# Kernel tuning notes

Hardware: AMD Instinct MI355X
Metric: run time of the kernel (lower is better)

The kernel has to match this reference:

```python
import jax, jax.numpy as jnp
import numpy as np

B, C, H, W = 8, 512, 32, 32
HEADS = 8
GROUPS = 32
EPS = 1e-5


def setup_inputs() -> dict:
    key = jax.random.key(0)
    ks = jax.random.split(key, 7)
    x = jax.random.normal(ks[0], (B, C, H, W), dtype=jnp.float32)
    gamma = jnp.ones((C,), dtype=jnp.float32)
    beta = jnp.zeros((C,), dtype=jnp.float32)
    w_qkv = jax.random.normal(ks[1], (3 * C, C), dtype=jnp.float32) * 0.02
    b_qkv = jnp.zeros((3 * C,), dtype=jnp.float32)
    # NOTE: original zero-inits proj; we use small random weights so the
    # attention path contributes to the output (zero proj => out == x).
    w_proj = jax.random.normal(ks[2], (C, C), dtype=jnp.float32) * 0.02
    b_proj = jnp.zeros((C,), dtype=jnp.float32)
    return {"x": x, "gamma": gamma, "beta": beta, "w_qkv": w_qkv,
            "b_qkv": b_qkv, "w_proj": w_proj, "b_proj": b_proj}


def group_norm(x, gamma, beta):
    b, c, h, w = x.shape
    xg = x.reshape(b, GROUPS, -1)
    mu = xg.mean(axis=-1, keepdims=True)
    var = xg.var(axis=-1, keepdims=True)
    xn = ((xg - mu) * jax.lax.rsqrt(var + EPS)).reshape(b, c, h, w)
    return xn * gamma[:, None, None] + beta[:, None, None]


def reference(x, gamma, beta, w_qkv, b_qkv, w_proj, b_proj):
    b, c, h, w = x.shape
    hd = c // HEADS
    n = h * w
    hn = group_norm(x, gamma, beta).reshape(b, c, n)        # [B,C,N]
    # 1x1 conv == channel matmul
    qkv = jnp.einsum('oc,bcn->bon', w_qkv, hn) + b_qkv[:, None]
    qkv = qkv.reshape(b, 3, HEADS, hd, n)
    q, k, v = qkv[:, 0], qkv[:, 1], qkv[:, 2]               # [B,H,hd,N]
    scale = hd ** -0.5
    scores = jnp.einsum('bhci,bhcj->bhij', q, k) * scale    # [B,H,N,N]
    attn = jax.nn.softmax(scores, axis=-1)                  # stable (max-sub)
    out = jnp.einsum('bhij,bhcj->bhci', attn, v).reshape(b, c, n)
    proj = jnp.einsum('oc,bcn->bon', w_proj, out) + b_proj[:, None]
    return x + proj.reshape(b, c, h, w)
```

## Files before the change

kernel.cpp:

```cpp
#include <hip/hip_runtime.h>
#include <math.h>

#define Bn 8
#define Cc 512
#define HW 1024
#define HEADS 8
#define HD 64
#define GROUPS 32
#define CPG 16
#define EPS 1e-5f

typedef float f32x4 __attribute__((ext_vector_type(4)));
typedef __bf16 bf16x8 __attribute__((ext_vector_type(8)));
typedef __bf16 bf16x4 __attribute__((ext_vector_type(4)));
typedef short s16x4 __attribute__((ext_vector_type(4)));
typedef unsigned u32x2 __attribute__((ext_vector_type(2)));

__device__ __forceinline__ void async16(const __bf16* g, __bf16* l) {
    __builtin_amdgcn_global_load_lds((const __attribute__((address_space(1))) unsigned int*)g,
                                     (__attribute__((address_space(3))) unsigned int*)l, 16, 0, 0);
}

__device__ __forceinline__ f32x4 mfma16(bf16x4 a, bf16x4 b, f32x4 c) {
    return __builtin_amdgcn_mfma_f32_16x16x16bf16_1k(
        __builtin_bit_cast(s16x4, a), __builtin_bit_cast(s16x4, b), c, 0, 0, 0);
}

__device__ __forceinline__ unsigned pk_bf16(float f1, float f0) {
    return __builtin_amdgcn_perm(__builtin_bit_cast(unsigned, f1),
                                 __builtin_bit_cast(unsigned, f0), 0x07060302u);
}

__global__ void conv_kernel(const float* __restrict__ a, __bf16* __restrict__ da, int na4,
                            const float* __restrict__ b, __bf16* __restrict__ db, int nb4) {
    int i = blockIdx.x * 256 + threadIdx.x;
    if (i < na4) {
        float4 v = ((const float4*)a)[i];
        bf16x4 o = { (__bf16)v.x, (__bf16)v.y, (__bf16)v.z, (__bf16)v.w };
        ((bf16x4*)da)[i] = o;
    } else {
        int j = i - na4;
        if (j < nb4) {
            float4 v = ((const float4*)b)[j];
            bf16x4 o = { (__bf16)v.x, (__bf16)v.y, (__bf16)v.z, (__bf16)v.w };
            ((bf16x4*)db)[j] = o;
        }
    }
}

__global__ __launch_bounds__(256) void gn_stats(const float* __restrict__ x,
                                                float* __restrict__ gstats) {
    int bg = blockIdx.x;
    int b = bg >> 5, g = bg & 31;
    const float* xp = x + ((size_t)b * Cc + g * CPG) * HW;
    int tid = threadIdx.x;
    float s = 0.f, ss = 0.f;
    for (int i = tid; i < CPG * HW; i += 256) {
        float v = xp[i];
        s += v; ss += v * v;
    }
    __shared__ float red0[4], red1[4];
    for (int off = 32; off > 0; off >>= 1) {
        s  += __shfl_down(s, off);
        ss += __shfl_down(ss, off);
    }
    int wave = tid >> 6, lane = tid & 63;
    if (lane == 0) { red0[wave] = s; red1[wave] = ss; }
    __syncthreads();
    if (tid == 0) {
        float S  = red0[0] + red0[1] + red0[2] + red0[3];
        float SS = red1[0] + red1[1] + red1[2] + red1[3];
        float mean = S / (float)(CPG * HW);
        float var  = SS / (float)(CPG * HW) - mean * mean;
        gstats[bg * 2]     = mean;
        gstats[bg * 2 + 1] = rsqrtf(var + EPS);
    }
}

__global__ __launch_bounds__(256) void gn_apply(const float* __restrict__ x,
                                                const float* __restrict__ gamma,
                                                const float* __restrict__ beta,
                                                const float* __restrict__ gstats,
                                                __bf16* __restrict__ hnT) {
    int b = blockIdx.y, n0 = blockIdx.x * 32;
    __shared__ __align__(16) __bf16 T[32 * 520];
    __shared__ float gl[512], bl[512], sm[32], sr[32];
    int tid = threadIdx.x;
    if (tid < 32) {
        sm[tid] = gstats[(b * 32 + tid) * 2];
        sr[tid] = gstats[(b * 32 + tid) * 2 + 1];
    }
    for (int i = tid; i < 512; i += 256) { gl[i] = gamma[i]; bl[i] = beta[i]; }
    __syncthreads();
    const float* xb = x + (size_t)b * Cc * HW + n0;
    for (int i = tid; i < 16384; i += 256) {
        int c = i >> 5, n = i & 31;
        float v = xb[(size_t)c * HW + n];
        int g = c >> 4;
        T[n * 520 + c] = (__bf16)((v - sm[g]) * sr[g] * gl[c] + bl[c]);
    }
    __syncthreads();
    __bf16* hb = hnT + ((size_t)b * HW + n0) * Cc;
    for (int j = tid; j < 2048; j += 256) {
        int n = j >> 6, ch = j & 63;
        *(bf16x8*)&hb[(size_t)n * Cc + ch * 8] = *(const bf16x8*)&T[n * 520 + ch * 8];
    }
}

__global__ __launch_bounds__(256) void qkv_gemm(
    const __bf16* __restrict__ hnT, const __bf16* __restrict__ wq,
    const float* __restrict__ bias, __bf16* __restrict__ qkT,
    __bf16* __restrict__ vbuf, float scaleLo) {
    __shared__ __align__(16) __bf16 As[128 * 64];
    __shared__ __align__(16) __bf16 Bs[128 * 64];
    int tid = threadIdx.x;
    int wv = tid >> 6, lane = tid & 63, ln = lane & 15, quad = lane >> 4;
    int b = blockIdx.z;
    bool isQK = blockIdx.y < 8;
    int bm = (isQK ? blockIdx.y : blockIdx.y - 8) * 128;
    int bn = blockIdx.x * 128;
    const __bf16* hb = hnT + (size_t)b * HW * Cc;
    const __bf16* Pb = isQK ? hb : wq + (size_t)1024 * 512;
    const __bf16* Qb = isQK ? wq : hb;
    int wm = (wv >> 1) * 64, wn = (wv & 1) * 64;

    f32x4 acc[4][4];
    #pragma unroll
    for (int i = 0; i < 4; ++i)
        #pragma unroll
        for (int j = 0; j < 4; ++j) acc[i][j] = (f32x4){0.f, 0.f, 0.f, 0.f};

    for (int k0 = 0; k0 < 512; k0 += 64) {
        __syncthreads();
        #pragma unroll
        for (int u = 0; u < 4; ++u) {
            int idx = u * 256 + tid;
            int r = idx >> 3, lc = idx & 7;
            int cg = lc ^ (r & 7);
            async16(Pb + (size_t)(bm + r) * 512 + k0 + cg * 8, &As[r * 64 + lc * 8]);
            async16(Qb + (size_t)(bn + r) * 512 + k0 + cg * 8, &Bs[r * 64 + lc * 8]);
        }
        __syncthreads();
        bf16x8 af[4][2], bff[4][2];
        #pragma unroll
        for (int mt = 0; mt < 4; ++mt) {
            int row = wm + mt * 16 + ln;
            #pragma unroll
            for (int h = 0; h < 2; ++h) {
                int cc = (h * 4 + quad) ^ (ln & 7);
                af[mt][h] = *(const bf16x8*)&As[row * 64 + cc * 8];
            }
        }
        #pragma unroll
        for (int nt = 0; nt < 4; ++nt) {
            int row = wn + nt * 16 + ln;
            #pragma unroll
            for (int h = 0; h < 2; ++h) {
                int cc = (h * 4 + quad) ^ (ln & 7);
                bff[nt][h] = *(const bf16x8*)&Bs[row * 64 + cc * 8];
            }
        }
        #pragma unroll
        for (int mt = 0; mt < 4; ++mt)
            #pragma unroll
            for (int nt = 0; nt < 4; ++nt) {
                acc[mt][nt] = __builtin_amdgcn_mfma_f32_16x16x32_bf16(af[mt][0], bff[nt][0], acc[mt][nt], 0, 0, 0);
                acc[mt][nt] = __builtin_amdgcn_mfma_f32_16x16x32_bf16(af[mt][1], bff[nt][1], acc[mt][nt], 0, 0, 0);
            }
    }

    if (isQK) {
        __bf16* out = qkT + (size_t)b * HW * 1024;
        float bcol[4], scol[4];
        #pragma unroll
        for (int nt = 0; nt < 4; ++nt) {
            int col = bn + wn + nt * 16 + ln;
            bcol[nt] = bias[col];
            scol[nt] = (col < 512) ? scaleLo : 1.0f;
        }
        #pragma unroll
        for (int mt = 0; mt < 4; ++mt)
            #pragma unroll
            for (int r = 0; r < 4; ++r) {
                int row = bm + wm + mt * 16 + quad * 4 + r;
                #pragma unroll
                for (int nt = 0; nt < 4; ++nt) {
                    int col = bn + wn + nt * 16 + ln;
                    out[(size_t)row * 1024 + col] = (__bf16)((acc[mt][nt][r] + bcol[nt]) * scol[nt]);
                }
            }
    } else {
        __bf16* out = vbuf + (size_t)b * Cc * HW;
        #pragma unroll
        for (int mt = 0; mt < 4; ++mt)
            #pragma unroll
            for (int r = 0; r < 4; ++r) {
                int row = bm + wm + mt * 16 + quad * 4 + r;
                float brow = bias[1024 + row];
                #pragma unroll
                for (int nt = 0; nt < 4; ++nt) {
                    int col = bn + wn + nt * 16 + ln;
                    out[(size_t)row * 1024 + col] = (__bf16)(acc[mt][nt][r] + brow);
                }
            }
    }
}

__global__ __launch_bounds__(256) void proj_gemm(
    const __bf16* __restrict__ wp, const __bf16* __restrict__ attnT,
    const float* __restrict__ bias, const float* __restrict__ resid,
    float* __restrict__ outp) {
    __shared__ __align__(16) __bf16 As[64 * 64];
    __shared__ __align__(16) __bf16 Bs[128 * 64];
    int tid = threadIdx.x;
    int wv = tid >> 6, lane = tid & 63, ln = lane & 15, quad = lane >> 4;
    int b = blockIdx.z;
    int bm = blockIdx.y * 64, bn = blockIdx.x * 128;
    const __bf16* Qb = attnT + (size_t)b * HW * Cc;
    int wm = (wv >> 1) * 32, wn = (wv & 1) * 64;

    f32x4 acc[2][4];
    #pragma unroll
    for (int i = 0; i < 2; ++i)
        #pragma unroll
        for (int j = 0; j < 4; ++j) acc[i][j] = (f32x4){0.f, 0.f, 0.f, 0.f};

    for (int k0 = 0; k0 < 512; k0 += 64) {
        __syncthreads();
        #pragma unroll
        for (int u = 0; u < 2; ++u) {
            int idx = u * 256 + tid;
            int r = idx >> 3, lc = idx & 7;
            int cg = lc ^ (r & 7);
            async16(wp + (size_t)(bm + r) * 512 + k0 + cg * 8, &As[r * 64 + lc * 8]);
        }
        #pragma unroll
        for (int u = 0; u < 4; ++u) {
            int idx = u * 256 + tid;
            int r = idx >> 3, lc = idx & 7;
            int cg = lc ^ (r & 7);
            async16(Qb + (size_t)(bn + r) * 512 + k0 + cg * 8, &Bs[r * 64 + lc * 8]);
        }
        __syncthreads();
        bf16x8 af[2][2], bff[4][2];
        #pragma unroll
        for (int mt = 0; mt < 2; ++mt) {
            int row = wm + mt * 16 + ln;
            #pragma unroll
            for (int h = 0; h < 2; ++h) {
                int cc = (h * 4 + quad) ^ (ln & 7);
                af[mt][h] = *(const bf16x8*)&As[row * 64 + cc * 8];
            }
        }
        #pragma unroll
        for (int nt = 0; nt < 4; ++nt) {
            int row = wn + nt * 16 + ln;
            #pragma unroll
            for (int h = 0; h < 2; ++h) {
                int cc = (h * 4 + quad) ^ (ln & 7);
                bff[nt][h] = *(const bf16x8*)&Bs[row * 64 + cc * 8];
            }
        }
        #pragma unroll
        for (int mt = 0; mt < 2; ++mt)
            #pragma unroll
            for (int nt = 0; nt < 4; ++nt) {
                acc[mt][nt] = __builtin_amdgcn_mfma_f32_16x16x32_bf16(af[mt][0], bff[nt][0], acc[mt][nt], 0, 0, 0);
                acc[mt][nt] = __builtin_amdgcn_mfma_f32_16x16x32_bf16(af[mt][1], bff[nt][1], acc[mt][nt], 0, 0, 0);
            }
    }

    float* out = outp + (size_t)b * Cc * HW;
    const float* res = resid + (size_t)b * Cc * HW;
    #pragma unroll
    for (int mt = 0; mt < 2; ++mt)
        #pragma unroll
        for (int r = 0; r < 4; ++r) {
            int row = bm + wm + mt * 16 + quad * 4 + r;
            float bv = bias[row];
            #pragma unroll
            for (int nt = 0; nt < 4; ++nt) {
                int col = bn + wn + nt * 16 + ln;
                size_t idx = (size_t)row * 1024 + col;
                out[idx] = acc[mt][nt][r] + bv + res[idx];
            }
        }
}

__global__ __launch_bounds__(256) void attn_mfma(const __bf16* __restrict__ qkT,
                                                 const __bf16* __restrict__ vbuf,
                                                 __bf16* __restrict__ attnT) {
    __shared__ __align__(16) __bf16 Ks[2][64 * 64];
    __shared__ __align__(16) __bf16 Vs[2][64 * 64];
    int tid = threadIdx.x;
    int wv = tid >> 6, lane = tid & 63, ln = lane & 15, quad = lane >> 4;
    int h = blockIdx.x, b = blockIdx.z;
    int i0 = blockIdx.y * 128 + wv * 32;

    const __bf16* qbase = qkT + ((size_t)b * HW + i0 + ln) * 1024 + h * HD + quad * 8;
    bf16x8 qf[2][2];
    #pragma unroll
    for (int mt = 0; mt < 2; ++mt) {
        qf[mt][0] = *(const bf16x8*)(qbase + (size_t)mt * 16 * 1024);
        qf[mt][1] = *(const bf16x8*)(qbase + (size_t)mt * 16 * 1024 + 32);
    }

    f32x4 oacc[2][4];
    #pragma unroll
    for (int mt = 0; mt < 2; ++mt)
        #pragma unroll
        for (int ct = 0; ct < 4; ++ct) oacc[mt][ct] = (f32x4){0.f, 0.f, 0.f, 0.f};
    float lsum[2] = {0.f, 0.f};

    for (int kt = 0; kt < 8; ++kt) {
        __syncthreads();
        #pragma unroll
        for (int hh = 0; hh < 2; ++hh) {
            int kb = kt * 128 + hh * 64;
            #pragma unroll
            for (int u = 0; u < 2; ++u) {
                int idx = u * 256 + tid;
                int r = idx >> 3, lc = idx & 7;
                int cg = lc ^ (r & 7);
                async16(qkT + ((size_t)b * HW + kb + r) * 1024 + 512 + h * HD + cg * 8,
                        &Ks[hh][idx * 8]);
                async16(vbuf + ((size_t)b * Cc + h * HD + r) * HW + kb + cg * 8,
                        &Vs[hh][idx * 8]);
            }
        }
        __syncthreads();

        #pragma unroll
        for (int hh = 0; hh < 2; ++hh) {
            f32x4 st[2][4];
            #pragma unroll
            for (int jt = 0; jt < 4; ++jt) {
                int row = jt * 16 + ln;
                int c0 = quad ^ (ln & 7);
                int c1 = (4 + quad) ^ (ln & 7);
                bf16x8 kf0 = *(const bf16x8*)&Ks[hh][row * 64 + c0 * 8];
                bf16x8 kf1 = *(const bf16x8*)&Ks[hh][row * 64 + c1 * 8];
                #pragma unroll
                for (int mt = 0; mt < 2; ++mt) {
                    f32x4 s = (f32x4){0.f, 0.f, 0.f, 0.f};
                    s = __builtin_amdgcn_mfma_f32_16x16x32_bf16(kf0, qf[mt][0], s, 0, 0, 0);
                    s = __builtin_amdgcn_mfma_f32_16x16x32_bf16(kf1, qf[mt][1], s, 0, 0, 0);
                    st[mt][jt] = s;
                }
            }

            bf16x4 pk[2][4];
            #pragma unroll
            for (int mt = 0; mt < 2; ++mt)
                #pragma unroll
                for (int jt = 0; jt < 4; ++jt) {
                    float p0 = __builtin_amdgcn_exp2f(st[mt][jt][0]);
                    float p1 = __builtin_amdgcn_exp2f(st[mt][jt][1]);
                    float p2 = __builtin_amdgcn_exp2f(st[mt][jt][2]);
                    float p3 = __builtin_amdgcn_exp2f(st[mt][jt][3]);
                    lsum[mt] += (p0 + p1) + (p2 + p3);
                    u32x2 w = { pk_bf16(p1, p0), pk_bf16(p3, p2) };
                    pk[mt][jt] = __builtin_bit_cast(bf16x4, w);
                }

            #pragma unroll
            for (int ct = 0; ct < 4; ++ct) {
                int row = ct * 16 + ln;
                bf16x4 vf[4];
                #pragma unroll
                for (int kss = 0; kss < 4; ++kss) {
                    int cc16 = (kss * 2 + (quad >> 1)) ^ (ln & 7);
                    vf[kss] = *(const bf16x4*)&Vs[hh][row * 64 + cc16 * 8 + (quad & 1) * 4];
                }
                #pragma unroll
                for (int mt = 0; mt < 2; ++mt)
                    #pragma unroll
                    for (int kss = 0; kss < 4; ++kss)
                        oacc[mt][ct] = mfma16(vf[kss], pk[mt][kss], oacc[mt][ct]);
            }
        }
    }

    #pragma unroll
    for (int mt = 0; mt < 2; ++mt) {
        lsum[mt] += __shfl_xor(lsum[mt], 16);
        lsum[mt] += __shfl_xor(lsum[mt], 32);
        float rl = 1.f / lsum[mt];
        __bf16* op = attnT + ((size_t)b * HW + i0 + mt * 16 + ln) * Cc + h * HD + quad * 4;
        #pragma unroll
        for (int ct = 0; ct < 4; ++ct) {
            bf16x4 o = { (__bf16)(oacc[mt][ct][0] * rl), (__bf16)(oacc[mt][ct][1] * rl),
                         (__bf16)(oacc[mt][ct][2] * rl), (__bf16)(oacc[mt][ct][3] * rl) };
            *(bf16x4*)(op + ct * 16) = o;
        }
    }
}

extern "C" void kernel_launch(void* const* d_in, const int* in_sizes, int n_in,
                              void* d_out, int out_size, void* d_ws, size_t ws_size,
                              hipStream_t stream) {
    const float* x      = (const float*)d_in[0];
    const float* gamma  = (const float*)d_in[1];
    const float* beta   = (const float*)d_in[2];
    const float* w_qkv  = (const float*)d_in[3];
    const float* b_qkv  = (const float*)d_in[4];
    const float* w_proj = (const float*)d_in[5];
    const float* b_proj = (const float*)d_in[6];
    float* out = (float*)d_out;

    __bf16* wq_bf  = (__bf16*)d_ws;
    __bf16* wp_bf  = wq_bf + (size_t)1536 * 512;
    __bf16* hnT    = wp_bf + (size_t)512 * 512;
    __bf16* qkT    = hnT + (size_t)Bn * HW * Cc;
    __bf16* vbuf   = qkT + (size_t)Bn * HW * 1024;
    __bf16* attnT  = vbuf + (size_t)Bn * Cc * HW;
    float*  gstats = (float*)(attnT + (size_t)Bn * HW * Cc);

    conv_kernel<<<1024, 256, 0, stream>>>(w_qkv, wq_bf, 196608, w_proj, wp_bf, 65536);

    gn_stats<<<Bn * GROUPS, 256, 0, stream>>>(x, gstats);
    dim3 gga(32, Bn);
    gn_apply<<<gga, 256, 0, stream>>>(x, gamma, beta, gstats, hnT);

    const float QSCALE = 0.125f * 1.44269504088896f;
    dim3 gqkv(8, 12, Bn);
    qkv_gemm<<<gqkv, 256, 0, stream>>>(hnT, wq_bf, b_qkv, qkT, vbuf, QSCALE);

    dim3 ga(8, 8, 8);
    attn_mfma<<<ga, 256, 0, stream>>>(qkT, vbuf, attnT);

    dim3 gp(8, 8, Bn);
    proj_gemm<<<gp, 256, 0, stream>>>(wp_bf, attnT, b_proj, x, out);
}
```

Before: 161.1 us.

## Fuse weight conversion with GN stats and halve attention query tile per block

```diff
diff --git a/kernel.cpp b/kernel.cpp
--- a/kernel.cpp
+++ b/kernel.cpp
@@ -31,29 +31,30 @@
                                  __builtin_bit_cast(unsigned, f0), 0x07060302u);
 }
 
-__global__ void conv_kernel(const float* __restrict__ a, __bf16* __restrict__ da, int na4,
-                            const float* __restrict__ b, __bf16* __restrict__ db, int nb4) {
-    int i = blockIdx.x * 256 + threadIdx.x;
-    if (i < na4) {
-        float4 v = ((const float4*)a)[i];
-        bf16x4 o = { (__bf16)v.x, (__bf16)v.y, (__bf16)v.z, (__bf16)v.w };
-        ((bf16x4*)da)[i] = o;
-    } else {
-        int j = i - na4;
-        if (j < nb4) {
-            float4 v = ((const float4*)b)[j];
+__global__ __launch_bounds__(256) void pre_kernel(const float* __restrict__ x,
+                                                  float* __restrict__ gstats,
+                                                  const float* __restrict__ wq,
+                                                  __bf16* __restrict__ wq_bf,
+                                                  const float* __restrict__ wp,
+                                                  __bf16* __restrict__ wp_bf) {
+    int blk = blockIdx.x;
+    int tid = threadIdx.x;
+    if (blk >= 256) {
+        int i = (blk - 256) * 256 + tid;
+        if (i < 196608) {
+            float4 v = ((const float4*)wq)[i];
             bf16x4 o = { (__bf16)v.x, (__bf16)v.y, (__bf16)v.z, (__bf16)v.w };
-            ((bf16x4*)db)[j] = o;
-        }
-    }
-}
-
-__global__ __launch_bounds__(256) void gn_stats(const float* __restrict__ x,
-                                                float* __restrict__ gstats) {
-    int bg = blockIdx.x;
-    int b = bg >> 5, g = bg & 31;
+            ((bf16x4*)wq_bf)[i] = o;
+        } else {
+            int j = i - 196608;
+            float4 v = ((const float4*)wp)[j];
+            bf16x4 o = { (__bf16)v.x, (__bf16)v.y, (__bf16)v.z, (__bf16)v.w };
+            ((bf16x4*)wp_bf)[j] = o;
+        }
+        return;
+    }
+    int b = blk >> 5, g = blk & 31;
     const float* xp = x + ((size_t)b * Cc + g * CPG) * HW;
-    int tid = threadIdx.x;
     float s = 0.f, ss = 0.f;
     for (int i = tid; i < CPG * HW; i += 256) {
         float v = xp[i];
@@ -72,8 +73,8 @@
         float SS = red1[0] + red1[1] + red1[2] + red1[3];
         float mean = S / (float)(CPG * HW);
         float var  = SS / (float)(CPG * HW) - mean * mean;
-        gstats[bg * 2]     = mean;
-        gstats[bg * 2 + 1] = rsqrtf(var + EPS);
+        gstats[blk * 2]     = mean;
+        gstats[blk * 2 + 1] = rsqrtf(var + EPS);
     }
 }
 
@@ -295,22 +296,16 @@
     int tid = threadIdx.x;
     int wv = tid >> 6, lane = tid & 63, ln = lane & 15, quad = lane >> 4;
     int h = blockIdx.x, b = blockIdx.z;
-    int i0 = blockIdx.y * 128 + wv * 32;
+    int i0 = blockIdx.y * 64 + wv * 16;
 
     const __bf16* qbase = qkT + ((size_t)b * HW + i0 + ln) * 1024 + h * HD + quad * 8;
-    bf16x8 qf[2][2];
+    bf16x8 qf0 = *(const bf16x8*)qbase;
+    bf16x8 qf1 = *(const bf16x8*)(qbase + 32);
+
+    f32x4 oacc[4];
     #pragma unroll
-    for (int mt = 0; mt < 2; ++mt) {
-        qf[mt][0] = *(const bf16x8*)(qbase + (size_t)mt * 16 * 1024);
-        qf[mt][1] = *(const bf16x8*)(qbase + (size_t)mt * 16 * 1024 + 32);
-    }
-
-    f32x4 oacc[2][4];
-    #pragma unroll
-    for (int mt = 0; mt < 2; ++mt)
-        #pragma unroll
-        for (int ct = 0; ct < 4; ++ct) oacc[mt][ct] = (f32x4){0.f, 0.f, 0.f, 0.f};
-    float lsum[2] = {0.f, 0.f};
+    for (int ct = 0; ct < 4; ++ct) oacc[ct] = (f32x4){0.f, 0.f, 0.f, 0.f};
+    float lsum = 0.f;
 
     for (int kt = 0; kt < 8; ++kt) {
         __syncthreads();
@@ -332,7 +327,7 @@
 
         #pragma unroll
         for (int hh = 0; hh < 2; ++hh) {
-            f32x4 st[2][4];
+            f32x4 st[4];
             #pragma unroll
             for (int jt = 0; jt < 4; ++jt) {
                 int row = jt * 16 + ln;
@@ -340,28 +335,23 @@
                 int c1 = (4 + quad) ^ (ln & 7);
                 bf16x8 kf0 = *(const bf16x8*)&Ks[hh][row * 64 + c0 * 8];
                 bf16x8 kf1 = *(const bf16x8*)&Ks[hh][row * 64 + c1 * 8];
-                #pragma unroll
-                for (int mt = 0; mt < 2; ++mt) {
-                    f32x4 s = (f32x4){0.f, 0.f, 0.f, 0.f};
-                    s = __builtin_amdgcn_mfma_f32_16x16x32_bf16(kf0, qf[mt][0], s, 0, 0, 0);
-                    s = __builtin_amdgcn_mfma_f32_16x16x32_bf16(kf1, qf[mt][1], s, 0, 0, 0);
-                    st[mt][jt] = s;
-                }
-            }
-
-            bf16x4 pk[2][4];
-            #pragma unroll
-            for (int mt = 0; mt < 2; ++mt)
-                #pragma unroll
-                for (int jt = 0; jt < 4; ++jt) {
-                    float p0 = __builtin_amdgcn_exp2f(st[mt][jt][0]);
-                    float p1 = __builtin_amdgcn_exp2f(st[mt][jt][1]);
-                    float p2 = __builtin_amdgcn_exp2f(st[mt][jt][2]);
-                    float p3 = __builtin_amdgcn_exp2f(st[mt][jt][3]);
-                    lsum[mt] += (p0 + p1) + (p2 + p3);
-                    u32x2 w = { pk_bf16(p1, p0), pk_bf16(p3, p2) };
-                    pk[mt][jt] = __builtin_bit_cast(bf16x4, w);
-                }
+                f32x4 s = (f32x4){0.f, 0.f, 0.f, 0.f};
+                s = __builtin_amdgcn_mfma_f32_16x16x32_bf16(kf0, qf0, s, 0, 0, 0);
+                s = __builtin_amdgcn_mfma_f32_16x16x32_bf16(kf1, qf1, s, 0, 0, 0);
+                st[jt] = s;
+            }
+
+            bf16x4 pk[4];
+            #pragma unroll
+            for (int jt = 0; jt < 4; ++jt) {
+                float p0 = __builtin_amdgcn_exp2f(st[jt][0]);
+                float p1 = __builtin_amdgcn_exp2f(st[jt][1]);
+                float p2 = __builtin_amdgcn_exp2f(st[jt][2]);
+                float p3 = __builtin_amdgcn_exp2f(st[jt][3]);
+                lsum += (p0 + p1) + (p2 + p3);
+                u32x2 w = { pk_bf16(p1, p0), pk_bf16(p3, p2) };
+                pk[jt] = __builtin_bit_cast(bf16x4, w);
+            }
 
             #pragma unroll
             for (int ct = 0; ct < 4; ++ct) {
@@ -373,26 +363,21 @@
                     vf[kss] = *(const bf16x4*)&Vs[hh][row * 64 + cc16 * 8 + (quad & 1) * 4];
                 }
                 #pragma unroll
-                for (int mt = 0; mt < 2; ++mt)
-                    #pragma unroll
-                    for (int kss = 0; kss < 4; ++kss)
-                        oacc[mt][ct] = mfma16(vf[kss], pk[mt][kss], oacc[mt][ct]);
-            }
-        }
-    }
-
+                for (int kss = 0; kss < 4; ++kss)
+                    oacc[ct] = mfma16(vf[kss], pk[kss], oacc[ct]);
+            }
+        }
+    }
+
+    lsum += __shfl_xor(lsum, 16);
+    lsum += __shfl_xor(lsum, 32);
+    float rl = 1.f / lsum;
+    __bf16* op = attnT + ((size_t)b * HW + i0 + ln) * Cc + h * HD + quad * 4;
     #pragma unroll
-    for (int mt = 0; mt < 2; ++mt) {
-        lsum[mt] += __shfl_xor(lsum[mt], 16);
-        lsum[mt] += __shfl_xor(lsum[mt], 32);
-        float rl = 1.f / lsum[mt];
-        __bf16* op = attnT + ((size_t)b * HW + i0 + mt * 16 + ln) * Cc + h * HD + quad * 4;
-        #pragma unroll
-        for (int ct = 0; ct < 4; ++ct) {
-            bf16x4 o = { (__bf16)(oacc[mt][ct][0] * rl), (__bf16)(oacc[mt][ct][1] * rl),
-                         (__bf16)(oacc[mt][ct][2] * rl), (__bf16)(oacc[mt][ct][3] * rl) };
-            *(bf16x4*)(op + ct * 16) = o;
-        }
+    for (int ct = 0; ct < 4; ++ct) {
+        bf16x4 o = { (__bf16)(oacc[ct][0] * rl), (__bf16)(oacc[ct][1] * rl),
+                     (__bf16)(oacc[ct][2] * rl), (__bf16)(oacc[ct][3] * rl) };
+        *(bf16x4*)(op + ct * 16) = o;
     }
 }
 
@@ -416,9 +401,8 @@
     __bf16* attnT  = vbuf + (size_t)Bn * Cc * HW;
     float*  gstats = (float*)(attnT + (size_t)Bn * HW * Cc);
 
-    conv_kernel<<<1024, 256, 0, stream>>>(w_qkv, wq_bf, 196608, w_proj, wp_bf, 65536);
-
-    gn_stats<<<Bn * GROUPS, 256, 0, stream>>>(x, gstats);
+    pre_kernel<<<1280, 256, 0, stream>>>(x, gstats, w_qkv, wq_bf, w_proj, wp_bf);
+
     dim3 gga(32, Bn);
     gn_apply<<<gga, 256, 0, stream>>>(x, gamma, beta, gstats, hnT);
 
@@ -426,7 +410,7 @@
     dim3 gqkv(8, 12, Bn);
     qkv_gemm<<<gqkv, 256, 0, stream>>>(hnT, wq_bf, b_qkv, qkT, vbuf, QSCALE);
 
-    dim3 ga(8, 8, 8);
+    dim3 ga(8, 16, 8);
     attn_mfma<<<ga, 256, 0, stream>>>(qkT, vbuf, attnT);
 
     dim3 gp(8, 8, Bn);
```

Result: no change. 164.0 us (+1.8%).

## Fuse weight conversion, group-norm stats and apply into one kernel

Applied to the files above, without the earlier changes.

```diff
diff --git a/kernel.cpp b/kernel.cpp
--- a/kernel.cpp
+++ b/kernel.cpp
@@ -31,35 +31,46 @@
                                  __builtin_bit_cast(unsigned, f0), 0x07060302u);
 }
 
-__global__ void conv_kernel(const float* __restrict__ a, __bf16* __restrict__ da, int na4,
-                            const float* __restrict__ b, __bf16* __restrict__ db, int nb4) {
-    int i = blockIdx.x * 256 + threadIdx.x;
-    if (i < na4) {
-        float4 v = ((const float4*)a)[i];
+__global__ __launch_bounds__(256) void gn_fused(const float* __restrict__ x,
+                                                const float* __restrict__ gamma,
+                                                const float* __restrict__ beta,
+                                                __bf16* __restrict__ hnT,
+                                                const float* __restrict__ wq,
+                                                __bf16* __restrict__ wq_bf,
+                                                const float* __restrict__ wp,
+                                                __bf16* __restrict__ wp_bf) {
+    int blk = blockIdx.x;
+    int tid = threadIdx.x;
+    if (blk >= 256) {
+        int i = (blk - 256) * 256 + tid;
+        if (i < 196608) {
+            float4 v = ((const float4*)wq)[i];
+            bf16x4 o = { (__bf16)v.x, (__bf16)v.y, (__bf16)v.z, (__bf16)v.w };
+            ((bf16x4*)wq_bf)[i] = o;
+        } else {
+            int j = i - 196608;
+            float4 v = ((const float4*)wp)[j];
+            bf16x4 o = { (__bf16)v.x, (__bf16)v.y, (__bf16)v.z, (__bf16)v.w };
+            ((bf16x4*)wp_bf)[j] = o;
+        }
+        return;
+    }
+    int b = blk >> 5, g = blk & 31;
+    const float* xp = x + ((size_t)b * Cc + g * CPG) * HW;
+
+    __shared__ __align__(16) __bf16 xs[16 * 1024];
+    __shared__ float red0[4], red1[4];
+    __shared__ float gls[16], bls[16], stats[2];
+    if (tid < 16) { gls[tid] = gamma[g * CPG + tid]; bls[tid] = beta[g * CPG + tid]; }
+
+    float s = 0.f, ss = 0.f;
+    for (int i4 = tid; i4 < 4096; i4 += 256) {
+        float4 v = ((const float4*)xp)[i4];
+        s  += (v.x + v.y) + (v.z + v.w);
+        ss += (v.x * v.x + v.y * v.y) + (v.z * v.z + v.w * v.w);
         bf16x4 o = { (__bf16)v.x, (__bf16)v.y, (__bf16)v.z, (__bf16)v.w };
-        ((bf16x4*)da)[i] = o;
-    } else {
-        int j = i - na4;
-        if (j < nb4) {
-            float4 v = ((const float4*)b)[j];
-            bf16x4 o = { (__bf16)v.x, (__bf16)v.y, (__bf16)v.z, (__bf16)v.w };
-            ((bf16x4*)db)[j] = o;
-        }
-    }
-}
-
-__global__ __launch_bounds__(256) void gn_stats(const float* __restrict__ x,
-                                                float* __restrict__ gstats) {
-    int bg = blockIdx.x;
-    int b = bg >> 5, g = bg & 31;
-    const float* xp = x + ((size_t)b * Cc + g * CPG) * HW;
-    int tid = threadIdx.x;
-    float s = 0.f, ss = 0.f;
-    for (int i = tid; i < CPG * HW; i += 256) {
-        float v = xp[i];
-        s += v; ss += v * v;
-    }
-    __shared__ float red0[4], red1[4];
+        ((bf16x4*)xs)[i4] = o;
+    }
     for (int off = 32; off > 0; off >>= 1) {
         s  += __shfl_down(s, off);
         ss += __shfl_down(ss, off);
@@ -72,38 +83,23 @@
         float SS = red1[0] + red1[1] + red1[2] + red1[3];
         float mean = S / (float)(CPG * HW);
         float var  = SS / (float)(CPG * HW) - mean * mean;
-        gstats[bg * 2]     = mean;
-        gstats[bg * 2 + 1] = rsqrtf(var + EPS);
-    }
-}
-
-__global__ __launch_bounds__(256) void gn_apply(const float* __restrict__ x,
-                                                const float* __restrict__ gamma,
-                                                const float* __restrict__ beta,
-                                                const float* __restrict__ gstats,
-                                                __bf16* __restrict__ hnT) {
-    int b = blockIdx.y, n0 = blockIdx.x * 32;
-    __shared__ __align__(16) __bf16 T[32 * 520];
-    __shared__ float gl[512], bl[512], sm[32], sr[32];
-    int tid = threadIdx.x;
-    if (tid < 32) {
-        sm[tid] = gstats[(b * 32 + tid) * 2];
-        sr[tid] = gstats[(b * 32 + tid) * 2 + 1];
-    }
-    for (int i = tid; i < 512; i += 256) { gl[i] = gamma[i]; bl[i] = beta[i]; }
+        stats[0] = mean;
+        stats[1] = rsqrtf(var + EPS);
+    }
     __syncthreads();
-    const float* xb = x + (size_t)b * Cc * HW + n0;
-    for (int i = tid; i < 16384; i += 256) {
-        int c = i >> 5, n = i & 31;
-        float v = xb[(size_t)c * HW + n];
-        int g = c >> 4;
-        T[n * 520 + c] = (__bf16)((v - sm[g]) * sr[g] * gl[c] + bl[c]);
-    }
-    __syncthreads();
-    __bf16* hb = hnT + ((size_t)b * HW + n0) * Cc;
-    for (int j = tid; j < 2048; j += 256) {
-        int n = j >> 6, ch = j & 63;
-        *(bf16x8*)&hb[(size_t)n * Cc + ch * 8] = *(const bf16x8*)&T[n * 520 + ch * 8];
+    float mean = stats[0], rstd = stats[1];
+    #pragma unroll
+    for (int u = 0; u < 4; ++u) {
+        int n = tid + u * 256;
+        union { __bf16 bs[16]; uint4 q[2]; } o;
+        #pragma unroll
+        for (int c = 0; c < 16; ++c) {
+            float v = (float)xs[c * 1024 + n];
+            o.bs[c] = (__bf16)((v - mean) * rstd * gls[c] + bls[c]);
+        }
+        uint4* dst = (uint4*)(hnT + ((size_t)b * HW + n) * Cc + g * CPG);
+        dst[0] = o.q[0];
+        dst[1] = o.q[1];
     }
 }
 
@@ -414,13 +410,8 @@
     __bf16* qkT    = hnT + (size_t)Bn * HW * Cc;
     __bf16* vbuf   = qkT + (size_t)Bn * HW * 1024;
     __bf16* attnT  = vbuf + (size_t)Bn * Cc * HW;
-    float*  gstats = (float*)(attnT + (size_t)Bn * HW * Cc);
-
-    conv_kernel<<<1024, 256, 0, stream>>>(w_qkv, wq_bf, 196608, w_proj, wp_bf, 65536);
-
-    gn_stats<<<Bn * GROUPS, 256, 0, stream>>>(x, gstats);
-    dim3 gga(32, Bn);
-    gn_apply<<<gga, 256, 0, stream>>>(x, gamma, beta, gstats, hnT);
+
+    gn_fused<<<1280, 256, 0, stream>>>(x, gamma, beta, hnT, w_qkv, wq_bf, w_proj, wp_bf);
 
     const float QSCALE = 0.125f * 1.44269504088896f;
     dim3 gqkv(8, 12, Bn);
```

Measured after the change: 146.0 us. 1.1x faster.
